# Performance work log

Measured on AMD Instinct MI355X. Metric: run time of the kernel, lower is better.

## Reference

```python
import jax, jax.numpy as jnp
import numpy as np
from jax import lax

B, L, D, H, V = 512, 60, 300, 256, 50000
NEG_INF = 10000.0  # the TF code uses -10000.0 as -inf in the mask


def setup_inputs() -> dict:
    key = jax.random.key(0)
    ks = jax.random.split(key, 18)
    s = 0.05
    rn = lambda k, shape: jax.random.normal(k, shape, jnp.float32) * s
    return {
        "E": rn(ks[0], (V, D)),
        "Wx1": rn(ks[1], (D, 4 * H)), "Wh1": rn(ks[2], (H, 4 * H)), "b1": jnp.zeros((4 * H,), jnp.float32),
        "Wx2": rn(ks[3], (D, 4 * H)), "Wh2": rn(ks[4], (H, 4 * H)), "b2": jnp.zeros((4 * H,), jnp.float32),
        "W_y": rn(ks[5], (H, H)), "Wh_a": rn(ks[6], (H, H)), "Wr_a": rn(ks[7], (H, H)),
        "w_a": rn(ks[8], (H,)), "Wt_a": rn(ks[9], (H, H)), "Wp_a": rn(ks[10], (H, H)), "Wxa": rn(ks[11], (H, H)),
        "U": rn(ks[12], (H, 2)), "b_out": jnp.zeros((1, 2), jnp.float32),
        "input1": jax.random.randint(ks[13], (B, L), 0, V, jnp.int32),
        "input2": jax.random.randint(ks[14], (B, L), 0, V, jnp.int32),
        "seqlen1": jax.random.randint(ks[15], (B,), 1, L + 1, jnp.int32),
        "seqlen2": jax.random.randint(ks[16], (B,), 1, L + 1, jnp.int32),
    }


def lstm_scan(x, seqlen, Wx, Wh, b):
    # TF BasicLSTMCell (forget_bias=1.0, gate order i,j,f,o) with dynamic_rnn
    # sequence_length semantics: past seqlen, output is 0 and state is frozen.
    Bsz = x.shape[0]
    h0 = jnp.zeros((Bsz, Wh.shape[0]), x.dtype)
    # precompute input projection for all timesteps: [L, B, 4H]
    xg = jnp.einsum('bld,dk->lbk', x, Wx) + b

    def step(carry, inputs):
        c, h = carry
        g_t, t = inputs
        gates = g_t + h @ Wh
        i, j, f, o = jnp.split(gates, 4, axis=-1)
        c_new = c * jax.nn.sigmoid(f + 1.0) + jax.nn.sigmoid(i) * jnp.tanh(j)
        h_new = jnp.tanh(c_new) * jax.nn.sigmoid(o)
        m = (t < seqlen)[:, None]
        return (jnp.where(m, c_new, c), jnp.where(m, h_new, h)), jnp.where(m, h_new, 0.0)

    (_, h_last), Y = lax.scan(step, (h0, h0), (xg, jnp.arange(x.shape[1])))
    return jnp.transpose(Y, (1, 0, 2)), h_last  # Y: [B, L, H]


def reference(E, Wx1, Wh1, b1, Wx2, Wh2, b2, W_y, Wh_a, Wr_a, w_a, Wt_a, Wp_a, Wxa,
              U, b_out, input1, input2, seqlen1, seqlen2):
    def mask_for(s):
        return jnp.where(jnp.arange(L)[None, :] < s[:, None], 0.0, -NEG_INF).astype(jnp.float32)

    def attend(Y, Y2, last_h, s2, mask1):
        # word-by-word attention (score_type=1 path):
        # M_t = tanh(W_y Y + (W_h h_t + W_r r_{t-1})), alpha_t = softmax(w.M_t + mask)
        # r_t = Y alpha_t + tanh(W_t r_{t-1})
        WyY = jnp.einsum('blh,hk->blk', Y, W_y)  # [B, L, H]
        r0 = jnp.zeros_like(last_h)

        def step(r, h_t):
            tmp = h_t @ Wh_a + r @ Wr_a                      # [B, H]
            M = jnp.tanh(WyY + tmp[:, None, :])              # [B, L, H]
            alpha = jax.nn.softmax(jnp.einsum('blh,h->bl', M, w_a) + mask1, axis=1)
            r_new = jnp.einsum('bl,blh->bh', alpha, Y) + jnp.tanh(r @ Wt_a)
            return r_new, r_new

        _, rs = lax.scan(step, r0, jnp.transpose(Y2, (1, 0, 2)))  # rs: [L, B, H]
        oh = jax.nn.one_hot(s2 - 1, L, dtype=Y.dtype)             # select r at last valid step
        r_L = jnp.einsum('bl,lbh->bh', oh, rs)
        return jnp.tanh(r_L @ Wp_a + last_h @ Wxa)

    def branch(tok1, tok2, s1, s2):
        x1, x2 = E[tok1], E[tok2]
        Y, _ = lstm_scan(x1, s1, Wx1, Wh1, b1)
        Y2, h2 = lstm_scan(x2, s2, Wx2, Wh2, b2)
        return attend(Y, Y2, h2, s2, mask_for(s1))

    last_h = branch(input1, input2, seqlen1, seqlen2) + branch(input2, input1, seqlen2, seqlen1)
    # dropout keep_prob = 1.0 (inference) -> identity
    return last_h @ U + b_out  # [B, 2]
```

## Files before the change

kernel.cpp:

```cpp
#include <hip/hip_runtime.h>
#include <cstdint>
#include <cstddef>

#define B_  512
#define L_  60
#define D_  300
#define H_  256
#define BT  1024
#define KX  320
#define KL  576
#define NG  1024
#define NBLK 512

typedef _Float16 half8   __attribute__((ext_vector_type(8)));
typedef _Float16 half4_t __attribute__((ext_vector_type(4)));
typedef float    floatx4 __attribute__((ext_vector_type(4)));

__device__ __forceinline__ float fast_tanh(float x){
    float e = __expf(2.f*x);
    return 1.f - 2.f*__builtin_amdgcn_rcpf(e + 1.f);
}
__device__ __forceinline__ float sigm(float x){
    return __builtin_amdgcn_rcpf(1.f + __expf(-x));
}

#define MFMA16(a,b,c) __builtin_amdgcn_mfma_f32_16x16x32_f16(a,b,c,0,0,0)

__global__ void k_fill4(uint4* __restrict__ p, int n4, uint32_t v){
    uint4 q = {v, v, v, v};
    int i = blockIdx.x*blockDim.x + threadIdx.x;
    int st = gridDim.x*blockDim.x;
    for (; i < n4; i += st) p[i] = q;
}

__global__ void k_sched(const int* __restrict__ s1, const int* __restrict__ s2,
                        int* __restrict__ perm)
{
    __shared__ int bins[61];
    __shared__ int base[61];
    const int tid = threadIdx.x;
    if (tid < 61) bins[tid] = 0;
    __syncthreads();
    int cap = (tid < B_) ? s2[tid] : s1[tid - B_];
    atomicAdd(&bins[cap], 1);
    __syncthreads();
    if (tid == 0) {
        int acc = 0;
        for (int c = 60; c >= 1; --c) { base[c] = acc; acc += bins[c]; }
    }
    __syncthreads();
    int pos = atomicAdd(&base[cap], 1);
    perm[pos] = tid;
}

__global__ __launch_bounds__(256, 2) void k_prep(
    const float* __restrict__ E,
    const float* __restrict__ Wx1, const float* __restrict__ Wh1,
    const float* __restrict__ Wx2, const float* __restrict__ Wh2,
    const float* __restrict__ W_y, const float* __restrict__ Wh_a, const float* __restrict__ Wr_a,
    const float* __restrict__ Wt_a, const float* __restrict__ Wp_a, const float* __restrict__ Wxa,
    const int* __restrict__ in1, const int* __restrict__ in2,
    _Float16* __restrict__ X16, _Float16* __restrict__ BcatT, _Float16* __restrict__ AW)
{
    const int tid = threadIdx.x;
    const int bid = blockIdx.x;

    for (int it = 0; it < 19; ++it) {
        int gid = it*131072 + bid*256 + tid;
        if (gid < 2457600) {
            int row = gid / (L_*40);
            int rem = gid - row*(L_*40);
            int t  = rem / 40;
            int ch = rem - t*40;
            int k0 = ch*8;
            int tok = (row < B_) ? in1[row*L_ + t] : in2[(row - B_)*L_ + t];
            const float* src = E + (size_t)tok*D_ + k0;
            half8 o;
            #pragma unroll
            for (int k = 0; k < 8; ++k) o[k] = (_Float16)0.f;
            if (k0 + 8 <= D_) {
                float4 a = *(const float4*)(src);
                float4 b = *(const float4*)(src + 4);
                o[0]=(_Float16)a.x; o[1]=(_Float16)a.y; o[2]=(_Float16)a.z; o[3]=(_Float16)a.w;
                o[4]=(_Float16)b.x; o[5]=(_Float16)b.y; o[6]=(_Float16)b.z; o[7]=(_Float16)b.w;
            } else if (k0 < D_) {
                float4 a = *(const float4*)(src);
                o[0]=(_Float16)a.x; o[1]=(_Float16)a.y; o[2]=(_Float16)a.z; o[3]=(_Float16)a.w;
            }
            *(half8*)(X16 + ((size_t)row*L_ + t)*KX + k0) = o;
        }
    }
    for (int it = 0; it < 9; ++it) {
        int idx = it*131072 + bid*256 + tid;
        int set = (idx >= KL*NG) ? 1 : 0;
        int rem = idx - set*(KL*NG);
        int k = rem >> 10, n = rem & 1023;
        const float* Wx = set ? Wx2 : Wx1;
        const float* Wh = set ? Wh2 : Wh1;
        float v = 0.f;
        if (k < D_)       v = Wx[k*NG + n];
        else if (k >= KX) v = Wh[(k - KX)*NG + n];
        BcatT[((size_t)set*NG + n)*KL + k] = (_Float16)v;
    }
    for (int it = 0; it < 4; ++it) {
        int idx = it*131072 + bid*256 + tid;
        if (idx < 458752) {
            float v; int dst;
            if (idx < 65536) {
                int k = idx >> 8, n = idx & 255;
                v = W_y[k*256 + n];
                dst = n*256 + k;
            } else if (idx < 131072) {
                int j = idx - 65536; int k = j >> 8, n = j & 255;
                v = Wh_a[k*256 + n];
                dst = 65536 + n*256 + k;
            } else if (idx < 262144) {
                int j = idx - 131072; int n = j >> 8, k = j & 255;
                v = (n < 256) ? Wr_a[k*256 + n] : Wt_a[k*256 + (n - 256)];
                dst = 131072 + n*256 + k;
            } else {
                int j = idx - 262144; int n = j >> 9, k = j & 511;
                v = (k < 256) ? Wp_a[k*256 + n] : Wxa[(k - 256)*256 + n];
                dst = 262144 + n*512 + k;
            }
            AW[dst] = (_Float16)v;
        }
    }
}

__global__ __launch_bounds__(256, 2) void k_lstm(
    const float* __restrict__ b1, const float* __restrict__ b2,
    const int* __restrict__ s1, const int* __restrict__ s2,
    const _Float16* __restrict__ X16, _Float16* __restrict__ Y16,
    const _Float16* __restrict__ BcatT,
    unsigned long long* __restrict__ hT, _Float16* __restrict__ hfin)
{
    __shared__ __align__(16) unsigned char shm[33792];

    const int tid = threadIdx.x;
    const int bid = blockIdx.x;
    const int lane = tid & 63, wv = tid >> 6;
    const int q = lane >> 4, lm = lane & 15;

    float (*sG)[64][65] = (float(*)[64][65])shm;
    _Float16* sA = (_Float16*)shm;

    const int ht = bid & 15, mt = bid >> 4;
    const int set = mt >> 4;
    const int m0 = mt*64;
    const int kh = wv >> 1;
    const int wn = (wv & 1)*32;
    const int cb = wn >> 4;

    half8 bfr[9][2];
    #pragma unroll
    for (int ch = 0; ch < 9; ++ch)
        #pragma unroll
        for (int ti = 0; ti < 2; ++ti) {
            bfr[ch][ti] = *(const half8*)(BcatT +
                ((size_t)set*NG + (cb+ti)*256 + ht*16 + lm)*KL + kh*288 + ch*32 + q*8);
            asm volatile("" : "+v"(bfr[ch][ti]));
        }

    const int amA = tid >> 2, kgA = (tid & 3)*8;
    const int pairA = kgA >> 1;
    const int rsA = (m0 + amA) & 1023;
    const int xrowA = set ? ((rsA + 512) & 1023) : rsA;

    const float* bias = set ? b2 : b1;
    const int pc = tid & 7;
    const int eh = ht*16 + pc*2;
    float bI[2], bJ[2], bF[2], bO[2];
    #pragma unroll
    for (int j = 0; j < 2; ++j) {
        bI[j] = bias[eh + j]; bJ[j] = bias[256 + eh + j];
        bF[j] = bias[512 + eh + j]; bO[j] = bias[768 + eh + j];
    }
    int esl[2]; float c_st[2][2], h_st[2][2];
    #pragma unroll
    for (int rp = 0; rp < 2; ++rp) {
        int rs = (m0 + (tid >> 3) + rp*32) & 1023;
        esl[rp] = (set == 0) ? ((rs < B_) ? s1[rs] : s2[rs - B_])
                             : ((rs < B_) ? s2[rs] : s1[rs - B_]);
        c_st[rp][0] = 0.f; c_st[rp][1] = 0.f;
        h_st[rp][0] = 0.f; h_st[rp][1] = 0.f;
    }

    half8 zero8;
    #pragma unroll
    for (int k = 0; k < 8; ++k) zero8[k] = (_Float16)0.f;

    for (int t = 0; t < L_; ++t) {
        const _Float16* aX = X16 + ((size_t)xrowA*L_ + t)*KX;
        const unsigned long long* hbase =
            hT + ((size_t)(((t - 1) & 1)*2 + set)*BT + rsA)*128;
        unsigned long long* hTo = hT + (size_t)((t & 1)*2 + set)*BT*128;
        const uint32_t wantTag = (uint32_t)(t - 1);

        floatx4 acc[4][2];
        #pragma unroll
        for (int mi = 0; mi < 4; ++mi)
            #pragma unroll
            for (int ti = 0; ti < 2; ++ti) acc[mi][ti] = (floatx4){0.f,0.f,0.f,0.f};

        half8 av0 = *(const half8*)(aX + kgA);
        half8 av1 = *(const half8*)(aX + 288 + kgA);
        unsigned long long hw[4];

        #pragma unroll
        for (int i = 0; i < 9; ++i) {
            __syncthreads();
            if (i > 0) {
                if (t > 0) {
                    const unsigned long long* hb = hbase + (i - 1)*16 + pairA;
                    #pragma unroll
                    for (int k = 0; k < 4; ++k) {
                        unsigned long long w = hw[k];
                        while ((uint32_t)(w >> 32) != wantTag)
                            w = __hip_atomic_load(hb + k, __ATOMIC_RELAXED,
                                                  __HIP_MEMORY_SCOPE_AGENT);
                        hw[k] = w;
                    }
                    union { uint32_t u[4]; half8 v; } cv;
                    #pragma unroll
                    for (int k = 0; k < 4; ++k) cv.u[k] = (uint32_t)hw[k];
                    av1 = cv.v;
                } else {
                    av1 = zero8;
                }
            }
            *(half8*)(sA + (     amA)*40 + kgA) = av0;
            *(half8*)(sA + (64 + amA)*40 + kgA) = av1;
            __syncthreads();
            if (i < 8) {
                av0 = *(const half8*)(aX + (i + 1)*32 + kgA);
                if (t > 0) {
                    const unsigned long long* hb = hbase + i*16 + pairA;
                    #pragma unroll
                    for (int k = 0; k < 4; ++k)
                        hw[k] = __hip_atomic_load(hb + k, __ATOMIC_RELAXED,
                                                  __HIP_MEMORY_SCOPE_AGENT);
                }
            }
            half8 af[4];
            #pragma unroll
            for (int mi = 0; mi < 4; ++mi)
                af[mi] = *(const half8*)(sA + (kh*64 + mi*16 + lm)*40 + q*8);
            #pragma unroll
            for (int mi = 0; mi < 4; ++mi) {
                acc[mi][0] = MFMA16(af[mi], bfr[i][0], acc[mi][0]);
                acc[mi][1] = MFMA16(af[mi], bfr[i][1], acc[mi][1]);
            }
        }

        __syncthreads();
        #pragma unroll
        for (int mi = 0; mi < 4; ++mi)
            #pragma unroll
            for (int ti = 0; ti < 2; ++ti)
                #pragma unroll
                for (int r = 0; r < 4; ++r)
                    sG[kh][mi*16 + q*4 + r][wn + ti*16 + lm] = acc[mi][ti][r];
        __syncthreads();

        #pragma unroll
        for (int rp = 0; rp < 2; ++rp) {
            int row = (tid >> 3) + rp*32;
            int gr = m0 + row;
            int rs = gr & 1023;
            bool act = (t < esl[rp]);
            union { _Float16 h[2]; uint32_t u; } hp, yp;
            #pragma unroll
            for (int j = 0; j < 2; ++j) {
                int hh = pc*2 + j;
                float gi = sG[0][row][     hh] + sG[1][row][     hh] + bI[j];
                float gj = sG[0][row][16 + hh] + sG[1][row][16 + hh] + bJ[j];
                float gf = sG[0][row][32 + hh] + sG[1][row][32 + hh] + bF[j];
                float go = sG[0][row][48 + hh] + sG[1][row][48 + hh] + bO[j];
                float c_new = c_st[rp][j]*sigm(gf + 1.f) + sigm(gi)*fast_tanh(gj);
                float h_new = fast_tanh(c_new)*sigm(go);
                if (act) { c_st[rp][j] = c_new; h_st[rp][j] = h_new; }
                hp.h[j] = (_Float16)h_st[rp][j];
                yp.h[j] = act ? (_Float16)h_new : (_Float16)0.f;
            }
            unsigned long long w = ((unsigned long long)(uint32_t)t << 32)
                                 | (unsigned long long)hp.u;
            __hip_atomic_store(hTo + (size_t)rs*128 + (eh >> 1), w,
                               __ATOMIC_RELAXED, __HIP_MEMORY_SCOPE_AGENT);
            if (set == 1 && t == L_ - 1)
                *(uint32_t*)(hfin + (size_t)rs*H_ + eh) = hp.u;
            *(uint32_t*)(Y16 + ((size_t)gr*L_ + t)*H_ + eh) = yp.u;
        }
    }
}

__global__ __launch_bounds__(256, 2) void k_wyth(
    const _Float16* __restrict__ Y16, _Float16* __restrict__ WyY16,
    _Float16* __restrict__ TH16, const _Float16* __restrict__ AW)
{
    __shared__ __align__(16) _Float16 sB[64*264];

    const int tid = threadIdx.x;
    const int bid = blockIdx.x;
    const int lane = tid & 63, wv = tid >> 6;
    const int q = lane >> 4, lm = lane & 15;

    const int slot = bid & 7;
    const int z = slot >> 2, nt = slot & 3;
    const int n0 = nt*64;
    {
        int rowB = tid >> 2;
        int kb = (tid & 3)*64;
        #pragma unroll
        for (int s = 0; s < 8; ++s)
            *(half8*)(sB + rowB*264 + kb + s*8) =
                *(const half8*)(AW + (size_t)z*65536 + (size_t)(n0 + rowB)*H_ + kb + s*8);
    }
    __syncthreads();
    const _Float16* Ybase = Y16 + (size_t)z*((size_t)BT*L_*H_);
    _Float16* dst = z ? TH16 : WyY16;
    for (int mi_ = 0; mi_ < 15; ++mi_) {
        int m0w = ((bid >> 3) + mi_*64)*64;
        floatx4 acc[4];
        #pragma unroll
        for (int ti = 0; ti < 4; ++ti) acc[ti] = (floatx4){0.f,0.f,0.f,0.f};
        const _Float16* aRow = Ybase + (size_t)(m0w + wv*16 + lm)*H_ + q*8;
        #pragma unroll
        for (int ch = 0; ch < 8; ++ch) {
            half8 a = *(const half8*)(aRow + ch*32);
            #pragma unroll
            for (int ti = 0; ti < 4; ++ti) {
                half8 b = *(const half8*)(sB + (ti*16 + lm)*264 + ch*32 + q*8);
                acc[ti] = MFMA16(a, b, acc[ti]);
            }
        }
        #pragma unroll
        for (int ti = 0; ti < 4; ++ti)
            #pragma unroll
            for (int r = 0; r < 4; ++r)
                dst[(size_t)(m0w + wv*16 + q*4 + r)*H_ + n0 + ti*16 + lm] = (_Float16)acc[ti][r];
    }
}

__global__ __launch_bounds__(512, 2) void k_att(
    const float* __restrict__ w_a, const int* __restrict__ s1, const int* __restrict__ s2,
    const _Float16* __restrict__ Y16, const _Float16* __restrict__ WyY16,
    const _Float16* __restrict__ TH16, const _Float16* __restrict__ AW,
    const int* __restrict__ perm, _Float16* __restrict__ rL16)
{
    __shared__ __align__(16) unsigned char shm[139520];

    _Float16* sY  = (_Float16*)shm;
    _Float16* sWy = (_Float16*)(shm + 61440);
    _Float16* sR  = (_Float16*)(shm + 124800);
    float*    sTW = (float*)(shm + 133248);
    float*    sWt = (float*)(shm + 135360);
    float*    sLog= (float*)(shm + 137408);
    float*    sAl = (float*)(shm + 137920);
    float*    sWa = (float*)(shm + 138432);
    int*      sU  = (int*)(shm + 139456);
    int*      sCap= (int*)(shm + 139464);
    int*      sAtt= (int*)(shm + 139472);

    const int tid = threadIdx.x;
    const int wv = tid >> 6, lane = tid & 63;
    const int q = lane >> 4, lm = lane & 15;

    if (tid < 2) {
        int u = perm[blockIdx.x*2 + tid];
        sU[tid] = u;
        sCap[tid] = (u < B_) ? s2[u] : s1[u - B_];
        sAtt[tid] = (u < B_) ? s1[u] : s2[u - B_];
    }
    __syncthreads();
    const int uA = sU[0], uB = sU[1];

    if (tid < 256) sWa[tid] = w_a[tid];
    for (int i = tid; i < 16*264; i += 512) sR[i] = (_Float16)0.f;
    for (int i = tid; i < 2*60*32; i += 512) {
        int row = i / 1920;
        int rem = i - row*1920;
        int l = rem >> 5, ch = rem & 31;
        int u = row ? uB : uA;
        *(half8*)(sY  + row*15360 + l*256 + ch*8) =
            *(const half8*)(Y16   + ((size_t)u*L_ + l)*H_ + ch*8);
        *(half8*)(sWy + row*15840 + l*264 + ch*8) =
            *(const half8*)(WyY16 + ((size_t)u*L_ + l)*H_ + ch*8);
    }
    half8 bfr[4][8];
    const _Float16* WrtT = AW + 131072;
    #pragma unroll
    for (int ti = 0; ti < 4; ++ti)
        #pragma unroll
        for (int ch = 0; ch < 8; ++ch) {
            bfr[ti][ch] = *(const half8*)(WrtT + (size_t)((wv*4 + ti)*16 + lm)*256 + ch*32 + q*8);
            asm volatile("" : "+v"(bfr[ti][ch]));
        }
    __syncthreads();

    const int cap0 = sCap[0], cap1 = sCap[1];
    const int att0 = sAtt[0], att1 = sAtt[1];
    const int mcap = max(cap0, cap1);

    const int rowB = wv >> 2, sB_ = wv & 3;
    const int lsub = lane >> 2, li = lane & 3;
    const int saB = rowB ? att1 : att0;
    const int rowD = tid >> 8, hD = tid & 255;
    const int capD = rowD ? cap1 : cap0;
    const int saD  = rowD ? att1 : att0;
    const int uD   = rowD ? uB : uA;

    const bool thl = (wv < 4) && (q == 0);
    const int  tc0 = (wv*4+0)*16 + lm, tc1 = (wv*4+1)*16 + lm,
               tc2 = (wv*4+2)*16 + lm, tc3 = (wv*4+3)*16 + lm;
    const _Float16* tb0 = TH16 + (size_t)uA*L_*H_;
    const _Float16* tb1 = TH16 + (size_t)uB*L_*H_;
    _Float16 thn[8];
    #pragma unroll
    for (int k = 0; k < 8; ++k) thn[k] = (_Float16)0.f;
    if (thl) {
        thn[0] = tb0[tc0]; thn[1] = tb0[tc1]; thn[2] = tb0[tc2]; thn[3] = tb0[tc3];
        thn[4] = tb1[tc0]; thn[5] = tb1[tc1]; thn[6] = tb1[tc2]; thn[7] = tb1[tc3];
    }

    for (int t = 0; t < mcap; ++t) {
        _Float16 thc[8];
        #pragma unroll
        for (int k = 0; k < 8; ++k) thc[k] = thn[k];
        if (thl && (t + 1 < mcap)) {
            const size_t o = (size_t)(t + 1)*H_;
            thn[0] = tb0[o + tc0]; thn[1] = tb0[o + tc1];
            thn[2] = tb0[o + tc2]; thn[3] = tb0[o + tc3];
            thn[4] = tb1[o + tc0]; thn[5] = tb1[o + tc1];
            thn[6] = tb1[o + tc2]; thn[7] = tb1[o + tc3];
        }
        floatx4 acc[4];
        #pragma unroll
        for (int ti = 0; ti < 4; ++ti) acc[ti] = (floatx4){0.f,0.f,0.f,0.f};
        #pragma unroll
        for (int ch = 0; ch < 8; ++ch) {
            half8 a = *(const half8*)(sR + lm*264 + ch*32 + q*8);
            #pragma unroll
            for (int ti = 0; ti < 4; ++ti)
                acc[ti] = MFMA16(a, bfr[ti][ch], acc[ti]);
        }
        if (q == 0) {
            if (wv < 4) {
                #pragma unroll
                for (int ti = 0; ti < 4; ++ti) {
                    int col = (wv*4 + ti)*16 + lm;
                    sTW[col]       = acc[ti][0] + (float)thc[ti];
                    sTW[264 + col] = acc[ti][1] + (float)thc[4 + ti];
                }
            } else {
                #pragma unroll
                for (int ti = 0; ti < 4; ++ti) {
                    int col = (wv*4 + ti)*16 + lm - 256;
                    sWt[col]       = fast_tanh(acc[ti][0]);
                    sWt[256 + col] = fast_tanh(acc[ti][1]);
                }
            }
        }
        __syncthreads();

        {
            int l = sB_*16 + lsub;
            float v = 0.f;
            if (l < saB) {
                const _Float16* wy = sWy + rowB*15840 + l*264;
                const float* tw = sTW + rowB*264;
                #pragma unroll
                for (int j = 0; j < 16; ++j) {
                    int h0 = j*16 + li*4;
                    half4_t yv = *(const half4_t*)(wy + h0);
                    #pragma unroll
                    for (int k = 0; k < 4; ++k)
                        v += fast_tanh((float)yv[k] + tw[h0 + k]) * sWa[h0 + k];
                }
            }
            v += __shfl_xor(v, 1);
            v += __shfl_xor(v, 2);
            if (li == 0 && l < saB) sLog[rowB*64 + l] = v;
        }
        __syncthreads();

        if (sB_ == 0) {
            float x = (lane < saB) ? sLog[rowB*64 + lane] : -3.4e38f;
            float m = x;
            #pragma unroll
            for (int off = 32; off > 0; off >>= 1) m = fmaxf(m, __shfl_xor(m, off));
            float e = (lane < saB) ? __expf(x - m) : 0.f;
            float ssum = e;
            #pragma unroll
            for (int off = 32; off > 0; off >>= 1) ssum += __shfl_xor(ssum, off);
            sAl[rowB*64 + lane] = e * __builtin_amdgcn_rcpf(ssum);
        }
        __syncthreads();

        if (t < capD) {
            float a_ = 0.f;
            const _Float16* yb = sY + rowD*15360 + hD;
            const float* al = sAl + rowD*64;
            #pragma unroll 4
            for (int l = 0; l < saD; ++l)
                a_ += al[l] * (float)yb[l*256];
            float rv = a_ + sWt[rowD*256 + hD];
            sR[rowD*264 + hD] = (_Float16)rv;
            if (t == capD - 1)
                rL16[(size_t)uD*H_ + hD] = (_Float16)rv;
        }
        __syncthreads();
    }
}

__global__ __launch_bounds__(256, 2) void k_ff(
    const _Float16* __restrict__ rL16, const _Float16* __restrict__ hfin,
    const _Float16* __restrict__ AW, float* __restrict__ ff)
{
    __shared__ __align__(16) unsigned char shm[10240];

    const int tid = threadIdx.x;
    const int bid = blockIdx.x;
    const int lane = tid & 63, wv = tid >> 6;
    const int q = lane >> 4, lm = lane & 15;

    _Float16* sA = (_Float16*)shm;
    _Float16* sB = (_Float16*)(shm + 5120);
    const _Float16* WfinT = AW + 262144;
    const int n0 = (bid & 3)*64, m0 = (bid >> 2)*64;
    const int wm = (wv & 1)*32, wn = (wv >> 1)*32;
    const int am = tid >> 2, kg = (tid & 3)*8;
    const int row = m0 + am;
    const _Float16* bRow = WfinT + (size_t)(n0 + am)*512;
    floatx4 acc00 = {0.f,0.f,0.f,0.f}, acc01 = acc00, acc10 = acc00, acc11 = acc00;
    for (int ch = 0; ch < 16; ++ch) {
        const int k0 = ch*32;
        half8 av = (k0 < 256) ? *(const half8*)(rL16 + (size_t)row*H_ + k0 + kg)
                              : *(const half8*)(hfin + (size_t)row*H_ + (k0 - 256) + kg);
        half8 bv = *(const half8*)(bRow + k0 + kg);
        __syncthreads();
        *(half8*)(sA + am*40 + kg) = av;
        *(half8*)(sB + am*40 + kg) = bv;
        __syncthreads();
        half8 a0v = *(const half8*)(sA + (wm + lm)*40 + q*8);
        half8 a1v = *(const half8*)(sA + (wm + 16 + lm)*40 + q*8);
        half8 b0v = *(const half8*)(sB + (wn + lm)*40 + q*8);
        half8 b1v = *(const half8*)(sB + (wn + 16 + lm)*40 + q*8);
        acc00 = MFMA16(a0v, b0v, acc00); acc01 = MFMA16(a0v, b1v, acc01);
        acc10 = MFMA16(a1v, b0v, acc10); acc11 = MFMA16(a1v, b1v, acc11);
    }
    int rb = m0 + wm + q*4, col = n0 + wn + lm;
    #pragma unroll
    for (int r = 0; r < 4; ++r) {
        ff[(size_t)(rb + r)*H_ + col]           = acc00[r];
        ff[(size_t)(rb + r)*H_ + col + 16]      = acc01[r];
        ff[(size_t)(rb + 16 + r)*H_ + col]      = acc10[r];
        ff[(size_t)(rb + 16 + r)*H_ + col + 16] = acc11[r];
    }
}

__global__ __launch_bounds__(256, 2) void k_out(
    const float* __restrict__ U, const float* __restrict__ b_o,
    const float* __restrict__ ff, float* __restrict__ out)
{
    __shared__ __align__(16) unsigned char shm[18432];

    const int tid = threadIdx.x;
    const int bid = blockIdx.x;
    const int lane = tid & 63, wv = tid >> 6;

    float* sTh = (float*)shm;
    float* sU  = (float*)(shm + 16384);
    const int b0 = bid*16;
    sU[tid] = U[tid]; sU[256 + tid] = U[256 + tid];
    for (int idx = tid; idx < 16*256; idx += 256) {
        int r = idx >> 8, h = idx & 255;
        sTh[idx] = fast_tanh(ff[(size_t)(b0 + r)*256 + h]) + fast_tanh(ff[(size_t)(b0 + r + 512)*256 + h]);
    }
    __syncthreads();
    for (int r = wv; r < 16; r += 4) {
        float p0 = 0.f, p1 = 0.f;
        #pragma unroll
        for (int k = 0; k < 4; ++k) {
            int h = lane*4 + k;
            float v = sTh[r*256 + h];
            p0 += v * sU[h*2];
            p1 += v * sU[h*2 + 1];
        }
        #pragma unroll
        for (int off = 32; off > 0; off >>= 1) { p0 += __shfl_down(p0, off); p1 += __shfl_down(p1, off); }
        if (lane == 0) {
            out[(b0 + r)*2]     = p0 + b_o[0];
            out[(b0 + r)*2 + 1] = p1 + b_o[1];
        }
    }
}

extern "C" void kernel_launch(void* const* d_in, const int* in_sizes, int n_in,
                              void* d_out, int out_size, void* d_ws, size_t ws_size,
                              hipStream_t stream)
{
    (void)in_sizes; (void)n_in; (void)out_size; (void)ws_size;
    const float* E    = (const float*)d_in[0];
    const float* Wx1  = (const float*)d_in[1];
    const float* Wh1  = (const float*)d_in[2];
    const float* b1   = (const float*)d_in[3];
    const float* Wx2  = (const float*)d_in[4];
    const float* Wh2  = (const float*)d_in[5];
    const float* b2   = (const float*)d_in[6];
    const float* W_y  = (const float*)d_in[7];
    const float* Wh_a = (const float*)d_in[8];
    const float* Wr_a = (const float*)d_in[9];
    const float* w_a  = (const float*)d_in[10];
    const float* Wt_a = (const float*)d_in[11];
    const float* Wp_a = (const float*)d_in[12];
    const float* Wxa  = (const float*)d_in[13];
    const float* U    = (const float*)d_in[14];
    const float* b_o  = (const float*)d_in[15];
    const int* in1 = (const int*)d_in[16];
    const int* in2 = (const int*)d_in[17];
    const int* s1  = (const int*)d_in[18];
    const int* s2  = (const int*)d_in[19];
    float* out = (float*)d_out;

    char* p = (char*)d_ws;
    auto alloc = [&](size_t bytes) { char* r = p; p += (bytes + 255) & ~(size_t)255; return r; };
    _Float16* X16   = (_Float16*)alloc((size_t)BT*L_*KX*2);
    _Float16* Y16   = (_Float16*)alloc(2ull*BT*L_*H_*2);
    _Float16* WyY16 = (_Float16*)alloc((size_t)BT*L_*H_*2);
    _Float16* TH16  = (_Float16*)alloc((size_t)BT*L_*H_*2);
    _Float16* BcatT = (_Float16*)alloc(2ull*NG*KL*2);
    _Float16* AW    = (_Float16*)alloc(393216ull*2);
    unsigned long long* hT = (unsigned long long*)alloc(4ull*BT*128*8);
    _Float16* hfin  = (_Float16*)alloc((size_t)BT*H_*2);
    _Float16* rL16  = (_Float16*)alloc((size_t)BT*H_*2);
    float*    ff    = (float*)   alloc((size_t)BT*H_*4);
    int*      perm  = (int*)     alloc(4096);

    k_fill4<<<256, 256, 0, stream>>>((uint4*)hT, (int)(4ull*BT*128*8/16), 0xFFFFFFFFu);
    k_sched<<<1, 1024, 0, stream>>>(s1, s2, perm);
    k_prep<<<NBLK, 256, 0, stream>>>(E, Wx1, Wh1, Wx2, Wh2,
        W_y, Wh_a, Wr_a, Wt_a, Wp_a, Wxa, in1, in2, X16, BcatT, AW);
    k_lstm<<<NBLK, 256, 0, stream>>>(b1, b2, s1, s2, X16, Y16, BcatT, hT, hfin);
    k_wyth<<<NBLK, 256, 0, stream>>>(Y16, WyY16, TH16, AW);
    k_att<<<512, 512, 0, stream>>>(w_a, s1, s2, Y16, WyY16, TH16, AW, perm, rL16);
    k_ff<<<64, 256, 0, stream>>>(rL16, hfin, AW, ff);
    k_out<<<32, 256, 0, stream>>>(U, b_o, ff, out);
}
```

Baseline: 1.083 ms.

## Reorder LSTM K-slabs so input projection precedes recurrent h loads

Permutes the K dimension of the concatenated weight matrix. The first five K-iterations now cover only the input projection, split into two halves, and the last four cover the recurrent h part. All h loads for the step are issued up front before the input MFMAs, so waiting on other blocks' tagged h values overlaps with the input-projection compute instead of stalling every slab. This raises register pressure (32 u64 values held live) and makes the weight layout more complex.

```diff
diff --git a/kernel.cpp b/kernel.cpp
--- a/kernel.cpp
+++ b/kernel.cpp
@@ -94,13 +94,18 @@
         int idx = it*131072 + bid*256 + tid;
         int set = (idx >= KL*NG) ? 1 : 0;
         int rem = idx - set*(KL*NG);
-        int k = rem >> 10, n = rem & 1023;
+        int kpos = rem >> 10, n = rem & 1023;
         const float* Wx = set ? Wx2 : Wx1;
         const float* Wh = set ? Wh2 : Wh1;
+        int half = (kpos >= 288) ? 1 : 0;
+        int rem2 = kpos - half*288;
+        int slab = rem2 >> 5, off = rem2 & 31;
+        int korig = (slab < 5) ? (slab*32 + half*160 + off)
+                               : (KX + (slab - 5)*64 + half*32 + off);
         float v = 0.f;
-        if (k < D_)       v = Wx[k*NG + n];
-        else if (k >= KX) v = Wh[(k - KX)*NG + n];
-        BcatT[((size_t)set*NG + n)*KL + k] = (_Float16)v;
+        if (korig < KX) { if (korig < D_) v = Wx[korig*NG + n]; }
+        else            v = Wh[(korig - KX)*NG + n];
+        BcatT[((size_t)set*NG + n)*KL + kpos] = (_Float16)v;
     }
     for (int it = 0; it < 4; ++it) {
         int idx = it*131072 + bid*256 + tid;
@@ -203,44 +208,57 @@
             #pragma unroll
             for (int ti = 0; ti < 2; ++ti) acc[mi][ti] = (floatx4){0.f,0.f,0.f,0.f};
 
+        unsigned long long hw0[4][4], hw1[4][4];
+        if (t > 0) {
+            #pragma unroll
+            for (int s = 0; s < 4; ++s)
+                #pragma unroll
+                for (int k = 0; k < 4; ++k) {
+                    hw0[s][k] = __hip_atomic_load(hbase + s*32 + pairA + k,
+                                                  __ATOMIC_RELAXED, __HIP_MEMORY_SCOPE_AGENT);
+                    hw1[s][k] = __hip_atomic_load(hbase + s*32 + 16 + pairA + k,
+                                                  __ATOMIC_RELAXED, __HIP_MEMORY_SCOPE_AGENT);
+                }
+        }
         half8 av0 = *(const half8*)(aX + kgA);
-        half8 av1 = *(const half8*)(aX + 288 + kgA);
-        unsigned long long hw[4];
+        half8 av1 = *(const half8*)(aX + 160 + kgA);
 
         #pragma unroll
         for (int i = 0; i < 9; ++i) {
             __syncthreads();
-            if (i > 0) {
+            if (i >= 5) {
                 if (t > 0) {
-                    const unsigned long long* hb = hbase + (i - 1)*16 + pairA;
+                    const int s = i - 5;
                     #pragma unroll
                     for (int k = 0; k < 4; ++k) {
-                        unsigned long long w = hw[k];
+                        unsigned long long w = hw0[s][k];
                         while ((uint32_t)(w >> 32) != wantTag)
-                            w = __hip_atomic_load(hb + k, __ATOMIC_RELAXED,
-                                                  __HIP_MEMORY_SCOPE_AGENT);
-                        hw[k] = w;
+                            w = __hip_atomic_load(hbase + s*32 + pairA + k,
+                                                  __ATOMIC_RELAXED, __HIP_MEMORY_SCOPE_AGENT);
+                        hw0[s][k] = w;
+                        unsigned long long w2 = hw1[s][k];
+                        while ((uint32_t)(w2 >> 32) != wantTag)
+                            w2 = __hip_atomic_load(hbase + s*32 + 16 + pairA + k,
+                                                   __ATOMIC_RELAXED, __HIP_MEMORY_SCOPE_AGENT);
+                        hw1[s][k] = w2;
                     }
-                    union { uint32_t u[4]; half8 v; } cv;
+                    union { uint32_t u[4]; half8 v; } c0, c1;
                     #pragma unroll
-                    for (int k = 0; k < 4; ++k) cv.u[k] = (uint32_t)hw[k];
-                    av1 = cv.v;
+                    for (int k = 0; k < 4; ++k) {
+                        c0.u[k] = (uint32_t)hw0[s][k];
+                        c1.u[k] = (uint32_t)hw1[s][k];
+                    }
+                    av0 = c0.v; av1 = c1.v;
                 } else {
-                    av1 = zero8;
+                    av0 = zero8; av1 = zero8;
                 }
             }
             *(half8*)(sA + (     amA)*40 + kgA) = av0;
             *(half8*)(sA + (64 + amA)*40 + kgA) = av1;
             __syncthreads();
-            if (i < 8) {
+            if (i < 4) {
                 av0 = *(const half8*)(aX + (i + 1)*32 + kgA);
-                if (t > 0) {
-                    const unsigned long long* hb = hbase + i*16 + pairA;
-                    #pragma unroll
-                    for (int k = 0; k < 4; ++k)
-                        hw[k] = __hip_atomic_load(hb + k, __ATOMIC_RELAXED,
-                                                  __HIP_MEMORY_SCOPE_AGENT);
-                }
+                av1 = *(const half8*)(aX + 160 + (i + 1)*32 + kgA);
             }
             half8 af[4];
             #pragma unroll
```

Result: slower. 1.513 ms (+39.6%).
